# Kernel tuning notes

Hardware: AMD Instinct MI355X
Metric: run time of the kernel (lower is better)

Reference implementation:

```python
import jax, jax.numpy as jnp
import numpy as np

H = 8        # heads
DH = 64      # dim_head
IMG = 32     # image_size
KS = 5       # kernel_size (odd)
SCALE = DH ** -0.5


def _unfold(t, ks):
    # t: (b, c, Hp, Wp) already padded. Returns (b, c*ks*ks, Ho*Wo) with
    # channel-major layout (c outermost, then kh, kw) matching torch F.unfold.
    b, c, Hp, Wp = t.shape
    Ho, Wo = Hp - ks + 1, Wp - ks + 1
    pat = jnp.stack([t[:, :, i:i + Ho, j:j + Wo]
                     for i in range(ks) for j in range(ks)], axis=2)  # (b,c,ks*ks,Ho,Wo)
    return pat.reshape(b, c * ks * ks, Ho * Wo)


def setup_inputs() -> dict:
    key = jax.random.key(0)
    k1, k2, k3, k4 = jax.random.split(key, 4)
    b, n, dim, inner = 2, 1152, 512, 512
    x = jax.random.normal(k1, (b, n, dim), jnp.float32)
    w_qkv = jax.random.normal(k2, (dim, inner * 3), jnp.float32) * 0.02
    w_out = jax.random.normal(k3, (inner, dim), jnp.float32) * 0.02
    b_out = jax.random.normal(k4, (dim,), jnp.float32) * 0.02
    return {"x": x, "w_qkv": w_qkv, "w_out": w_out, "b_out": b_out}


def reference(x, w_qkv, w_out, b_out):
    b, n, dim = x.shape
    img_len = IMG * IMG
    text_len = n - img_len
    NEG = -jnp.finfo(x.dtype).max

    qkv = x @ w_qkv                                   # (b, n, 3*inner)
    q, k, v = jnp.split(qkv, 3, axis=-1)

    def to_heads(t):
        return t.reshape(b, n, H, DH).transpose(0, 2, 1, 3).reshape(b * H, n, DH)

    q = to_heads(q) * SCALE
    k = to_heads(k)
    v = to_heads(v)

    # faithful to source: text slice is t[:, img_seq_len:], image is t[:, -img_seq_len:]
    q_text, q_img = q[:, img_len:], q[:, -img_len:]
    k_text, k_img = k[:, img_len:], k[:, -img_len:]
    v_text, v_img = v[:, img_len:], v[:, -img_len:]

    # ---- text branch. NOTE: source uses non-inplace masked_fill, so the
    # causal mask has NO effect -> plain softmax (faithful reproduction).
    dots_text = jnp.einsum('bid,bjd->bij', q_text, k_text)
    attn_text = jax.nn.softmax(dots_text, axis=-1)
    out_text = jnp.einsum('bij,bjd->bid', attn_text, v_text)

    # ---- image branch: local window via unfold
    def to_loc(t):
        g = t.transpose(0, 2, 1).reshape(b * H, DH, IMG, IMG)
        p = KS // 2
        g = jnp.pad(g, ((0, 0), (0, 0), (p, p), (p, p)))
        u = _unfold(g, KS)  # (bh, DH*KS*KS, img_len), channel-major (d outer)
        # faithful to source rearrange 'b (j d) i -> b i j d' (j outermost),
        # which regroups the channel-major unfold output.
        return u.reshape(b * H, KS * KS, DH, img_len).transpose(0, 3, 1, 2)

    k_loc = to_loc(k_img)  # (bh, img_len, KS*KS, DH)
    v_loc = to_loc(v_img)

    dots_txt = jnp.einsum('bid,bjd->bij', q_img, k_text)     # (bh, img_len, text_len)
    dots_loc = jnp.einsum('bid,bijd->bij', q_img, k_loc)     # (bh, img_len, KS*KS)

    # per-query key index mask (padded positions get index img_len -> never masked)
    p = KS // 2
    idx = jnp.arange(img_len, dtype=jnp.float32).reshape(1, 1, IMG, IMG)
    idx = jnp.pad(idx, ((0, 0), (0, 0), (p, p), (p, p)), constant_values=float(img_len))
    kidx = _unfold(idx, KS).transpose(0, 2, 1)               # (1, img_len, KS*KS)
    qidx = jnp.arange(img_len, dtype=jnp.float32).reshape(1, -1, 1)
    mask_loc = qidx <= kidx                                  # faithful: keep q <= k
    dots_loc = jnp.where(mask_loc, dots_loc, NEG)

    dots_img = jnp.concatenate([dots_txt, dots_loc], axis=-1)
    attn_img = jax.nn.softmax(dots_img, axis=-1)
    out_img = (jnp.einsum('bij,bjd->bid', attn_img[..., :text_len], v_text)
               + jnp.einsum('bij,bijd->bid', attn_img[..., text_len:], v_loc))

    out = jnp.concatenate([out_text, out_img], axis=1)       # (bh, n, DH)
    out = out.reshape(b, H, n, DH).transpose(0, 2, 1, 3).reshape(b, n, H * DH)
    return out @ w_out + b_out
```

## Files before the change

kernel.cpp:

```cpp
#include <hip/hip_runtime.h>
#include <hip/hip_bf16.h>
#include <math.h>

#define NTOK 1152
#define DIM 512
#define NQKV 1536
#define DHEAD 64
#define NBH 16
#define TEXTN 128
#define IMGLEN 1024
#define SEG (NBH * NTOK * DHEAD)
#define STF 68
#define TSTATE_F (NBH * IMGLEN * STF)
#define LPAD 40
#define KTSZ (NBH * TEXTN * DHEAD)

typedef __attribute__((ext_vector_type(8))) short bf16x8;
typedef __attribute__((ext_vector_type(4))) float f32x4;

__device__ __forceinline__ ushort f2bf(float f) {
    unsigned u = __float_as_uint(f);
    unsigned r = (u + 0x7FFFu + ((u >> 16) & 1u)) >> 16;
    return (ushort)r;
}
__device__ __forceinline__ float bf2f(ushort u) {
    return __uint_as_float(((unsigned)u) << 16);
}

__global__ __launch_bounds__(256) void prep_x_k(const float* __restrict__ X,
                                                ushort* __restrict__ xhi,
                                                ushort* __restrict__ xlo) {
    int i = (blockIdx.x * 256 + threadIdx.x) * 4;
    float4 v = *(const float4*)(X + i);
    ushort4 h, l;
    h.x = f2bf(v.x); l.x = f2bf(v.x - bf2f(h.x));
    h.y = f2bf(v.y); l.y = f2bf(v.y - bf2f(h.y));
    h.z = f2bf(v.z); l.z = f2bf(v.z - bf2f(h.z));
    h.w = f2bf(v.w); l.w = f2bf(v.w - bf2f(h.w));
    *(ushort4*)(xhi + i) = h;
    *(ushort4*)(xlo + i) = l;
}

__global__ __launch_bounds__(256) void prep_wt_k(const float* __restrict__ W,
                                                 ushort* __restrict__ thi,
                                                 ushort* __restrict__ tlo,
                                                 int K, int N) {
    __shared__ float tile[32][33];
    const int bx = blockIdx.x, by = blockIdx.y;
    const int c = threadIdx.x & 31, r8 = threadIdx.x >> 5;
#pragma unroll
    for (int i = 0; i < 4; ++i) {
        int rr = r8 + i * 8;
        tile[rr][c] = W[(size_t)(by * 32 + rr) * N + bx * 32 + c];
    }
    __syncthreads();
#pragma unroll
    for (int i = 0; i < 4; ++i) {
        int rr = r8 + i * 8;
        float v = tile[c][rr];
        size_t o = (size_t)(bx * 32 + rr) * K + by * 32 + c;
        ushort h = f2bf(v);
        thi[o] = h;
        tlo[o] = f2bf(v - bf2f(h));
    }
}

__global__ __launch_bounds__(256) void gemm_qkv_mfma(const ushort* __restrict__ xhi,
                                                     const ushort* __restrict__ xlo,
                                                     const ushort* __restrict__ wthi,
                                                     const ushort* __restrict__ wtlo,
                                                     float* __restrict__ qh,
                                                     float* __restrict__ kh,
                                                     float* __restrict__ vh,
                                                     ushort* __restrict__ qhi,
                                                     ushort* __restrict__ qlo,
                                                     ushort* __restrict__ kthi,
                                                     ushort* __restrict__ ktlo,
                                                     ushort* __restrict__ vthi,
                                                     ushort* __restrict__ vtlo) {
    __shared__ __align__(16) ushort Ah[128 * LPAD], Al[128 * LPAD];
    __shared__ __align__(16) ushort Bh[64 * LPAD], Bl[64 * LPAD];
    const int tid = threadIdx.x;
    const int lane = tid & 63;
    const int w = tid >> 6;
    const int wm = w >> 1, wn = w & 1;
    const int row0 = blockIdx.y * 128;
    const int col0 = blockIdx.x * 64;

    f32x4 acc[4][2];
#pragma unroll
    for (int a = 0; a < 4; ++a)
#pragma unroll
        for (int b = 0; b < 2; ++b) acc[a][b] = (f32x4){0.f, 0.f, 0.f, 0.f};

    const int arow = tid >> 1;
    const int akb = (tid & 1) * 16;
    const int brow = tid >> 2;
    const int bkb = (tid & 3) * 8;
    const int kf = (lane >> 4) * 8;
    const int lr = lane & 15;

    for (int k0 = 0; k0 < DIM; k0 += 32) {
        {
            const size_t g = (size_t)(row0 + arow) * DIM + k0 + akb;
            *(bf16x8*)&Ah[arow * LPAD + akb] = *(const bf16x8*)(xhi + g);
            *(bf16x8*)&Ah[arow * LPAD + akb + 8] = *(const bf16x8*)(xhi + g + 8);
            *(bf16x8*)&Al[arow * LPAD + akb] = *(const bf16x8*)(xlo + g);
            *(bf16x8*)&Al[arow * LPAD + akb + 8] = *(const bf16x8*)(xlo + g + 8);
        }
        {
            const size_t g = (size_t)(col0 + brow) * DIM + k0 + bkb;
            *(bf16x8*)&Bh[brow * LPAD + bkb] = *(const bf16x8*)(wthi + g);
            *(bf16x8*)&Bl[brow * LPAD + bkb] = *(const bf16x8*)(wtlo + g);
        }
        __syncthreads();
        bf16x8 ah[4], al[4], bh[2], bl[2];
#pragma unroll
        for (int mi = 0; mi < 4; ++mi) {
            int rr = wm * 64 + mi * 16 + lr;
            ah[mi] = *(const bf16x8*)&Ah[rr * LPAD + kf];
            al[mi] = *(const bf16x8*)&Al[rr * LPAD + kf];
        }
#pragma unroll
        for (int ni = 0; ni < 2; ++ni) {
            int rr = wn * 32 + ni * 16 + lr;
            bh[ni] = *(const bf16x8*)&Bh[rr * LPAD + kf];
            bl[ni] = *(const bf16x8*)&Bl[rr * LPAD + kf];
        }
#pragma unroll
        for (int mi = 0; mi < 4; ++mi)
#pragma unroll
            for (int ni = 0; ni < 2; ++ni) {
                acc[mi][ni] = __builtin_amdgcn_mfma_f32_16x16x32_bf16(ah[mi], bh[ni], acc[mi][ni], 0, 0, 0);
                acc[mi][ni] = __builtin_amdgcn_mfma_f32_16x16x32_bf16(ah[mi], bl[ni], acc[mi][ni], 0, 0, 0);
                acc[mi][ni] = __builtin_amdgcn_mfma_f32_16x16x32_bf16(al[mi], bh[ni], acc[mi][ni], 0, 0, 0);
            }
        __syncthreads();
    }

    const int which = col0 >> 9;
    const int hh = (col0 & 511) >> 6;
    const float scale = (which == 0) ? 0.125f : 1.f;
    float* dst = (which == 0) ? qh : ((which == 1) ? kh : vh);
#pragma unroll
    for (int mi = 0; mi < 4; ++mi)
#pragma unroll
        for (int ni = 0; ni < 2; ++ni)
#pragma unroll
            for (int j = 0; j < 4; ++j) {
                int r = row0 + wm * 64 + mi * 16 + (lane >> 4) * 4 + j;
                int b_i = r / NTOK, tok = r - b_i * NTOK;
                int d = wn * 32 + ni * 16 + (lane & 15);
                int bhi = b_i * 8 + hh;
                float val = acc[mi][ni][j] * scale;
                dst[((size_t)bhi * NTOK + tok) * DHEAD + d] = val;
                if (which == 0) {
                    size_t qo = ((size_t)bhi * NTOK + tok) * DHEAD + d;
                    ushort h2 = f2bf(val);
                    qhi[qo] = h2;
                    qlo[qo] = f2bf(val - bf2f(h2));
                } else if (tok >= IMGLEN) {
                    int tr = tok - IMGLEN;
                    ushort h2 = f2bf(val);
                    ushort l2 = f2bf(val - bf2f(h2));
                    if (which == 1) {
                        size_t ko = ((size_t)bhi * TEXTN + tr) * DHEAD + d;
                        kthi[ko] = h2; ktlo[ko] = l2;
                    } else {
                        size_t vo = ((size_t)bhi * DHEAD + d) * TEXTN + tr;
                        vthi[vo] = h2; vtlo[vo] = l2;
                    }
                }
            }
}

__global__ __launch_bounds__(256) void attn_text_mfma(const ushort* __restrict__ qhi,
                                                      const ushort* __restrict__ qlo,
                                                      const ushort* __restrict__ kthi,
                                                      const ushort* __restrict__ ktlo,
                                                      const ushort* __restrict__ vthi,
                                                      const ushort* __restrict__ vtlo,
                                                      ushort* __restrict__ ahi,
                                                      ushort* __restrict__ alo,
                                                      float* __restrict__ tstate) {
    __shared__ __align__(16) ushort Phi[4][16][136];
    __shared__ __align__(16) ushort Plo[4][16][136];
    const int bh = blockIdx.x / 18;
    const int tile = blockIdx.x % 18;
    const int wave = threadIdx.x >> 6;
    const int lane = threadIdx.x & 63;
    const int lr = lane & 15, lg = lane >> 4;
    const int kf = lg * 8;
    const int qrow0 = tile * 64 + wave * 16;
    const int tok0 = (tile < 2 ? 1024 + tile * 64 : tile * 64) + wave * 16;

    bf16x8 qah[2], qal[2];
    {
        const size_t qb = ((size_t)bh * NTOK + tok0 + lr) * DHEAD;
#pragma unroll
        for (int c = 0; c < 2; ++c) {
            qah[c] = *(const bf16x8*)(qhi + qb + c * 32 + kf);
            qal[c] = *(const bf16x8*)(qlo + qb + c * 32 + kf);
        }
    }
    f32x4 s[8];
#pragma unroll
    for (int t = 0; t < 8; ++t) s[t] = (f32x4){0.f, 0.f, 0.f, 0.f};
#pragma unroll
    for (int t = 0; t < 8; ++t) {
        const size_t kb = ((size_t)bh * TEXTN + t * 16 + lr) * DHEAD;
#pragma unroll
        for (int c = 0; c < 2; ++c) {
            bf16x8 kbh = *(const bf16x8*)(kthi + kb + c * 32 + kf);
            bf16x8 kbl = *(const bf16x8*)(ktlo + kb + c * 32 + kf);
            s[t] = __builtin_amdgcn_mfma_f32_16x16x32_bf16(qah[c], kbh, s[t], 0, 0, 0);
            s[t] = __builtin_amdgcn_mfma_f32_16x16x32_bf16(qah[c], kbl, s[t], 0, 0, 0);
            s[t] = __builtin_amdgcn_mfma_f32_16x16x32_bf16(qal[c], kbh, s[t], 0, 0, 0);
        }
    }
    float mx[4], sm[4];
#pragma unroll
    for (int r = 0; r < 4; ++r) {
        float v = s[0][r];
#pragma unroll
        for (int t = 1; t < 8; ++t) v = fmaxf(v, s[t][r]);
        mx[r] = v;
    }
#pragma unroll
    for (int msk = 1; msk <= 8; msk <<= 1)
#pragma unroll
        for (int r = 0; r < 4; ++r) mx[r] = fmaxf(mx[r], __shfl_xor(mx[r], msk));
#pragma unroll
    for (int r = 0; r < 4; ++r) sm[r] = 0.f;
#pragma unroll
    for (int t = 0; t < 8; ++t)
#pragma unroll
        for (int r = 0; r < 4; ++r) {
            float p = __expf(s[t][r] - mx[r]);
            s[t][r] = p;
            sm[r] += p;
        }
#pragma unroll
    for (int msk = 1; msk <= 8; msk <<= 1)
#pragma unroll
        for (int r = 0; r < 4; ++r) sm[r] += __shfl_xor(sm[r], msk);
#pragma unroll
    for (int t = 0; t < 8; ++t)
#pragma unroll
        for (int r = 0; r < 4; ++r) {
            float p = s[t][r];
            ushort h = f2bf(p);
            Phi[wave][lg * 4 + r][t * 16 + lr] = h;
            Plo[wave][lg * 4 + r][t * 16 + lr] = f2bf(p - bf2f(h));
        }
    __syncthreads();
    f32x4 o[4];
#pragma unroll
    for (int dt = 0; dt < 4; ++dt) o[dt] = (f32x4){0.f, 0.f, 0.f, 0.f};
#pragma unroll
    for (int c = 0; c < 4; ++c) {
        bf16x8 pah = *(const bf16x8*)&Phi[wave][lr][c * 32 + kf];
        bf16x8 pal = *(const bf16x8*)&Plo[wave][lr][c * 32 + kf];
#pragma unroll
        for (int dt = 0; dt < 4; ++dt) {
            const size_t vb = ((size_t)bh * DHEAD + dt * 16 + lr) * TEXTN + c * 32 + kf;
            bf16x8 vbh = *(const bf16x8*)(vthi + vb);
            bf16x8 vbl = *(const bf16x8*)(vtlo + vb);
            o[dt] = __builtin_amdgcn_mfma_f32_16x16x32_bf16(pah, vbh, o[dt], 0, 0, 0);
            o[dt] = __builtin_amdgcn_mfma_f32_16x16x32_bf16(pah, vbl, o[dt], 0, 0, 0);
            o[dt] = __builtin_amdgcn_mfma_f32_16x16x32_bf16(pal, vbh, o[dt], 0, 0, 0);
        }
    }
    if (tile < 2) {
#pragma unroll
        for (int r = 0; r < 4; ++r) {
            const int row = qrow0 + lg * 4 + r;
            const float inv = 1.f / sm[r];
            const size_t base = ((size_t)bh * NTOK + row) * DHEAD;
#pragma unroll
            for (int dt = 0; dt < 4; ++dt) {
                float v = o[dt][r] * inv;
                ushort h = f2bf(v);
                ahi[base + dt * 16 + lr] = h;
                alo[base + dt * 16 + lr] = f2bf(v - bf2f(h));
            }
        }
    } else {
#pragma unroll
        for (int r = 0; r < 4; ++r) {
            const int imgq = qrow0 - TEXTN + lg * 4 + r;
            float* st = tstate + ((size_t)bh * IMGLEN + imgq) * STF;
#pragma unroll
            for (int dt = 0; dt < 4; ++dt) st[dt * 16 + lr] = o[dt][r];
            if (lr == 0) { st[64] = mx[r]; st[65] = sm[r]; }
        }
    }
}

template <int W8>
__device__ inline void loc_dots8(const float* __restrict__ kimg, int y, int x,
                                 const float (&q)[64], float (&sd)[25]) {
#pragma unroll
    for (int t = 0; t < 25; ++t) {
        const int ny = y + t / 5 - 2;
        const int nx = x + t % 5 - 2;
        if (ny >= 0 && ny < 32 && nx >= 0 && nx < 32) {
            const float* kp = kimg + (size_t)(ny * 32 + nx) * DHEAD + W8 * 8;
            float4 k0 = *(const float4*)kp;
            float4 k1 = *(const float4*)(kp + 4);
            float ke[8] = {k0.x, k0.y, k0.z, k0.w, k1.x, k1.y, k1.z, k1.w};
#pragma unroll
            for (int e = 0; e < 8; ++e) {
                const int d = W8 * 8 + e;
                const int id2 = d * 25 + t;
                sd[id2 >> 6] += q[id2 & 63] * ke[e];
            }
        }
    }
}

template <int W, int T0, int T1>
__device__ inline void loc_pvr(const float* __restrict__ vimg, int y, int x,
                               const float (&p)[25], float (&po)[64]) {
#pragma unroll
    for (int t = T0; t < T1; ++t) {
        const int ny = y + t / 5 - 2;
        const int nx = x + t % 5 - 2;
        if (ny >= 0 && ny < 32 && nx >= 0 && nx < 32) {
            const float* vp = vimg + (size_t)(ny * 32 + nx) * DHEAD + W * 16;
#pragma unroll
            for (int g = 0; g < 4; ++g) {
                float4 vv = *(const float4*)(vp + g * 4);
                float ve[4] = {vv.x, vv.y, vv.z, vv.w};
#pragma unroll
                for (int e = 0; e < 4; ++e) {
                    const int d = W * 16 + g * 4 + e;
                    const int id2 = d * 25 + t;
                    po[id2 & 63] += p[id2 >> 6] * ve[e];
                }
            }
        }
    }
}

__global__ __launch_bounds__(512) void attn_img_k(const float* __restrict__ qh,
                                                  const float* __restrict__ kh,
                                                  const float* __restrict__ vh,
                                                  ushort* __restrict__ ahi,
                                                  ushort* __restrict__ alo,
                                                  const float* __restrict__ tstate) {
    __shared__ __align__(16) float smem[8 * 64 * 26];
    float (*sdb)[64][26] = reinterpret_cast<float (*)[64][26]>(smem);
    float (*pob)[64][68] = reinterpret_cast<float (*)[64][68]>(smem);
    const int bh = blockIdx.x >> 4;
    const int qtile = (blockIdx.x & 15) << 6;
    const int wave = threadIdx.x >> 6;
    const int lane = threadIdx.x & 63;
    const int qq = qtile + lane;
    const int y = qq >> 5, x = qq & 31;
    const float* kimg = kh + (size_t)(bh * NTOK + TEXTN) * DHEAD;
    const float* vimg = vh + (size_t)(bh * NTOK + TEXTN) * DHEAD;
    const float* st = tstate + ((size_t)(bh * IMGLEN + qq)) * STF;

    float sd[25];
#pragma unroll
    for (int j = 0; j < 25; ++j) sd[j] = 0.f;
    {
        float q[64];
        const float* qp = qh + ((size_t)(bh * NTOK + TEXTN + qq)) * DHEAD;
#pragma unroll
        for (int g = 0; g < 16; ++g) {
            float4 v4 = *(const float4*)(qp + g * 4);
            q[g * 4] = v4.x; q[g * 4 + 1] = v4.y; q[g * 4 + 2] = v4.z; q[g * 4 + 3] = v4.w;
        }
        switch (wave) {
            case 0: loc_dots8<0>(kimg, y, x, q, sd); break;
            case 1: loc_dots8<1>(kimg, y, x, q, sd); break;
            case 2: loc_dots8<2>(kimg, y, x, q, sd); break;
            case 3: loc_dots8<3>(kimg, y, x, q, sd); break;
            case 4: loc_dots8<4>(kimg, y, x, q, sd); break;
            case 5: loc_dots8<5>(kimg, y, x, q, sd); break;
            case 6: loc_dots8<6>(kimg, y, x, q, sd); break;
            default: loc_dots8<7>(kimg, y, x, q, sd); break;
        }
    }
#pragma unroll
    for (int j = 0; j < 25; ++j) sdb[wave][lane][j] = sd[j];
    __syncthreads();

    float p[25];
#pragma unroll
    for (int j = 0; j < 25; ++j)
        p[j] = ((sdb[0][lane][j] + sdb[1][lane][j]) + (sdb[2][lane][j] + sdb[3][lane][j])) +
               ((sdb[4][lane][j] + sdb[5][lane][j]) + (sdb[6][lane][j] + sdb[7][lane][j]));
    float m = st[64], l = st[65];
    float mloc = -1e30f;
#pragma unroll
    for (int j = 0; j < 25; ++j) {
        const int my = y + j / 5 - 2;
        const int mx = x + j % 5 - 2;
        bool inb = (my >= 0 && my < 32 && mx >= 0 && mx < 32);
        bool keep = inb ? (qq <= my * 32 + mx) : true;
        p[j] = keep ? p[j] : -1e30f;
        mloc = fmaxf(mloc, p[j]);
    }
    const float M = fmaxf(m, mloc);
    const float cc = __expf(m - M);
    l *= cc;
#pragma unroll
    for (int j = 0; j < 25; ++j) {
        p[j] = __expf(p[j] - M);
        l += p[j];
    }
    const float inv = 1.f / l;

    float po[64];
#pragma unroll
    for (int o = 0; o < 64; ++o) po[o] = 0.f;
    switch (wave) {
        case 0: loc_pvr<0, 0, 13>(vimg, y, x, p, po); break;
        case 1: loc_pvr<1, 0, 13>(vimg, y, x, p, po); break;
        case 2: loc_pvr<2, 0, 13>(vimg, y, x, p, po); break;
        case 3: loc_pvr<3, 0, 13>(vimg, y, x, p, po); break;
        case 4: loc_pvr<0, 13, 25>(vimg, y, x, p, po); break;
        case 5: loc_pvr<1, 13, 25>(vimg, y, x, p, po); break;
        case 6: loc_pvr<2, 13, 25>(vimg, y, x, p, po); break;
        default: loc_pvr<3, 13, 25>(vimg, y, x, p, po); break;
    }
    __syncthreads();

    if (wave < 2) {
#pragma unroll
        for (int o = 0; o < 64; ++o) pob[wave][lane][o] = po[o];
    }
    __syncthreads();
    if (wave >= 2 && wave < 4) {
#pragma unroll
        for (int o = 0; o < 64; ++o) pob[wave - 2][lane][o] += po[o];
    }
    __syncthreads();
    if (wave >= 4 && wave < 6) {
#pragma unroll
        for (int o = 0; o < 64; ++o) pob[wave - 4][lane][o] += po[o];
    }
    __syncthreads();
    if (wave >= 6) {
#pragma unroll
        for (int o = 0; o < 64; ++o) pob[wave - 6][lane][o] += po[o];
    }
    __syncthreads();

    if (wave < 4) {
        const float* stq = st + wave * 16;
        size_t base = ((size_t)(bh * NTOK + TEXTN + qq)) * DHEAD + wave * 16;
#pragma unroll
        for (int g = 0; g < 4; ++g) {
            float4 tv = *(const float4*)(stq + g * 4);
            float4 a0 = *(const float4*)&pob[0][lane][wave * 16 + g * 4];
            float4 a1 = *(const float4*)&pob[1][lane][wave * 16 + g * 4];
            float v0 = (a0.x + a1.x + cc * tv.x) * inv;
            float v1 = (a0.y + a1.y + cc * tv.y) * inv;
            float v2 = (a0.z + a1.z + cc * tv.z) * inv;
            float v3 = (a0.w + a1.w + cc * tv.w) * inv;
            ushort4 oh, ol;
            oh.x = f2bf(v0); ol.x = f2bf(v0 - bf2f(oh.x));
            oh.y = f2bf(v1); ol.y = f2bf(v1 - bf2f(oh.y));
            oh.z = f2bf(v2); ol.z = f2bf(v2 - bf2f(oh.z));
            oh.w = f2bf(v3); ol.w = f2bf(v3 - bf2f(oh.w));
            *(ushort4*)(ahi + base + g * 4) = oh;
            *(ushort4*)(alo + base + g * 4) = ol;
        }
    }
}

__global__ __launch_bounds__(256) void gemm_out_mfma(const ushort* __restrict__ ahi,
                                                     const ushort* __restrict__ alo,
                                                     const ushort* __restrict__ wthi,
                                                     const ushort* __restrict__ wtlo,
                                                     const float* __restrict__ bias,
                                                     float* __restrict__ Y) {
    __shared__ __align__(16) ushort Ah[128 * LPAD], Al[128 * LPAD];
    __shared__ __align__(16) ushort Bh[64 * LPAD], Bl[64 * LPAD];
    const int tid = threadIdx.x;
    const int lane = tid & 63;
    const int w = tid >> 6;
    const int wm = w >> 1, wn = w & 1;
    const int row0 = blockIdx.y * 128;
    const int col0 = blockIdx.x * 64;

    f32x4 acc[4][2];
#pragma unroll
    for (int a = 0; a < 4; ++a)
#pragma unroll
        for (int b = 0; b < 2; ++b) acc[a][b] = (f32x4){0.f, 0.f, 0.f, 0.f};

    const int arow = tid >> 1;
    const int akb = (tid & 1) * 16;
    const int brow = tid >> 2;
    const int bkb = (tid & 3) * 8;
    const int kf = (lane >> 4) * 8;
    const int lr = lane & 15;

    const int ar = row0 + arow;
    const int a_bi = ar / NTOK;
    const int a_tok = ar - a_bi * NTOK;

    for (int k0 = 0; k0 < DIM; k0 += 32) {
        {
            const int kg = k0 + akb;
            const int hh = kg >> 6, d0 = kg & 63;
            const size_t g = ((size_t)(a_bi * 8 + hh) * NTOK + a_tok) * DHEAD + d0;
            *(bf16x8*)&Ah[arow * LPAD + akb] = *(const bf16x8*)(ahi + g);
            *(bf16x8*)&Ah[arow * LPAD + akb + 8] = *(const bf16x8*)(ahi + g + 8);
            *(bf16x8*)&Al[arow * LPAD + akb] = *(const bf16x8*)(alo + g);
            *(bf16x8*)&Al[arow * LPAD + akb + 8] = *(const bf16x8*)(alo + g + 8);
        }
        {
            const size_t g = (size_t)(col0 + brow) * DIM + k0 + bkb;
            *(bf16x8*)&Bh[brow * LPAD + bkb] = *(const bf16x8*)(wthi + g);
            *(bf16x8*)&Bl[brow * LPAD + bkb] = *(const bf16x8*)(wtlo + g);
        }
        __syncthreads();
        bf16x8 ah[4], al[4], bh[2], bl[2];
#pragma unroll
        for (int mi = 0; mi < 4; ++mi) {
            int rr = wm * 64 + mi * 16 + lr;
            ah[mi] = *(const bf16x8*)&Ah[rr * LPAD + kf];
            al[mi] = *(const bf16x8*)&Al[rr * LPAD + kf];
        }
#pragma unroll
        for (int ni = 0; ni < 2; ++ni) {
            int rr = wn * 32 + ni * 16 + lr;
            bh[ni] = *(const bf16x8*)&Bh[rr * LPAD + kf];
            bl[ni] = *(const bf16x8*)&Bl[rr * LPAD + kf];
        }
#pragma unroll
        for (int mi = 0; mi < 4; ++mi)
#pragma unroll
            for (int ni = 0; ni < 2; ++ni) {
                acc[mi][ni] = __builtin_amdgcn_mfma_f32_16x16x32_bf16(ah[mi], bh[ni], acc[mi][ni], 0, 0, 0);
                acc[mi][ni] = __builtin_amdgcn_mfma_f32_16x16x32_bf16(ah[mi], bl[ni], acc[mi][ni], 0, 0, 0);
                acc[mi][ni] = __builtin_amdgcn_mfma_f32_16x16x32_bf16(al[mi], bh[ni], acc[mi][ni], 0, 0, 0);
            }
        __syncthreads();
    }

#pragma unroll
    for (int mi = 0; mi < 4; ++mi)
#pragma unroll
        for (int ni = 0; ni < 2; ++ni) {
            int cidx = col0 + wn * 32 + ni * 16 + (lane & 15);
            float bv = bias[cidx];
#pragma unroll
            for (int j = 0; j < 4; ++j) {
                int r = row0 + wm * 64 + mi * 16 + (lane >> 4) * 4 + j;
                Y[(size_t)r * DIM + cidx] = acc[mi][ni][j] + bv;
            }
        }
}

extern "C" void kernel_launch(void* const* d_in, const int* in_sizes, int n_in,
                              void* d_out, int out_size, void* d_ws, size_t ws_size,
                              hipStream_t stream) {
    const float* x = (const float*)d_in[0];
    const float* w_qkv = (const float*)d_in[1];
    const float* w_out = (const float*)d_in[2];
    const float* b_out = (const float*)d_in[3];
    float* Y = (float*)d_out;
    float* ws = (float*)d_ws;
    float* qh = ws;
    float* kh = ws + (size_t)SEG;
    float* vh = ws + 2 * (size_t)SEG;
    float* tstate = ws + 3 * (size_t)SEG;
    ushort* xhi = (ushort*)(ws + 3 * (size_t)SEG + TSTATE_F);
    ushort* xlo = xhi + (size_t)SEG;
    ushort* ahi = xhi;
    ushort* alo = xlo;
    ushort* wqthi = xlo + (size_t)SEG;
    ushort* wqtlo = wqthi + (size_t)DIM * NQKV;
    ushort* wothi = wqtlo + (size_t)DIM * NQKV;
    ushort* wotlo = wothi + (size_t)DIM * DIM;
    ushort* qhi = wotlo + (size_t)DIM * DIM;
    ushort* qlo = qhi + (size_t)SEG;
    ushort* kthi = qlo + (size_t)SEG;
    ushort* ktlo = kthi + (size_t)KTSZ;
    ushort* vthi = ktlo + (size_t)KTSZ;
    ushort* vtlo = vthi + (size_t)KTSZ;

    hipLaunchKernelGGL(prep_x_k, dim3(SEG / 1024), dim3(256), 0, stream, x, xhi, xlo);
    hipLaunchKernelGGL(prep_wt_k, dim3(NQKV / 32, DIM / 32), dim3(256), 0, stream,
                       w_qkv, wqthi, wqtlo, DIM, NQKV);
    hipLaunchKernelGGL(prep_wt_k, dim3(DIM / 32, DIM / 32), dim3(256), 0, stream,
                       w_out, wothi, wotlo, DIM, DIM);
    hipLaunchKernelGGL(gemm_qkv_mfma, dim3(NQKV / 64, 2304 / 128), dim3(256), 0, stream,
                       xhi, xlo, wqthi, wqtlo, qh, kh, vh,
                       qhi, qlo, kthi, ktlo, vthi, vtlo);
    hipLaunchKernelGGL(attn_text_mfma, dim3(NBH * 18), dim3(256), 0, stream,
                       qhi, qlo, kthi, ktlo, vthi, vtlo, ahi, alo, tstate);
    hipLaunchKernelGGL(attn_img_k, dim3(NBH * 16), dim3(512), 0, stream,
                       qh, kh, vh, ahi, alo, tstate);
    hipLaunchKernelGGL(gemm_out_mfma, dim3(DIM / 64, 2304 / 128), dim3(256), 0, stream,
                       ahi, alo, wothi, wotlo, b_out, Y);
}
```

Measured before the change: 133.6 us.

## Stage local-window K/V halo tiles in swizzled LDS for image attention

The image local-attention kernel now cooperatively loads a 6-row halo of K and V (192 pixels) plus the block's Q tile into shared memory, using an XOR swizzle to avoid bank conflicts. The window dot products and PV accumulation then read from LDS instead of re-reading global memory for each of the 25 neighbours. This removes redundant global and cache traffic. In exchange, LDS use grows to roughly 150KB per block, so launch bounds are pinned to one block per CU, which reduces occupancy.

```diff
diff --git a/kernel.cpp b/kernel.cpp
--- a/kernel.cpp
+++ b/kernel.cpp
@@ -298,16 +298,17 @@
 }
 
 template <int W8>
-__device__ inline void loc_dots8(const float* __restrict__ kimg, int y, int x,
-                                 const float (&q)[64], float (&sd)[25]) {
+__device__ inline void loc_dots8_lds(const float* __restrict__ Kl, int yloc, int x, int y,
+                                     const float (&q)[64], float (&sd)[25]) {
 #pragma unroll
     for (int t = 0; t < 25; ++t) {
         const int ny = y + t / 5 - 2;
         const int nx = x + t % 5 - 2;
         if (ny >= 0 && ny < 32 && nx >= 0 && nx < 32) {
-            const float* kp = kimg + (size_t)(ny * 32 + nx) * DHEAD + W8 * 8;
-            float4 k0 = *(const float4*)kp;
-            float4 k1 = *(const float4*)(kp + 4);
+            const int px = (yloc + t / 5) * 32 + nx;
+            const float* base = Kl + px * 64;
+            float4 k0 = *(const float4*)(base + (((2 * W8) ^ (px & 7)) << 2));
+            float4 k1 = *(const float4*)(base + (((2 * W8 + 1) ^ (px & 7)) << 2));
             float ke[8] = {k0.x, k0.y, k0.z, k0.w, k1.x, k1.y, k1.z, k1.w};
 #pragma unroll
             for (int e = 0; e < 8; ++e) {
@@ -320,69 +321,97 @@
 }
 
 template <int W, int T0, int T1>
-__device__ inline void loc_pvr(const float* __restrict__ vimg, int y, int x,
-                               const float (&p)[25], float (&po)[64]) {
+__device__ inline void loc_pvr_lds(const float* __restrict__ Vl, int yloc, int x, int y,
+                                   const float (&pp)[25], float (&po)[64]) {
 #pragma unroll
     for (int t = T0; t < T1; ++t) {
         const int ny = y + t / 5 - 2;
         const int nx = x + t % 5 - 2;
         if (ny >= 0 && ny < 32 && nx >= 0 && nx < 32) {
-            const float* vp = vimg + (size_t)(ny * 32 + nx) * DHEAD + W * 16;
+            const int px = (yloc + t / 5) * 32 + nx;
+            const float* base = Vl + px * 64;
 #pragma unroll
             for (int g = 0; g < 4; ++g) {
-                float4 vv = *(const float4*)(vp + g * 4);
+                float4 vv = *(const float4*)(base + (((4 * W + g) ^ (px & 7)) << 2));
                 float ve[4] = {vv.x, vv.y, vv.z, vv.w};
 #pragma unroll
                 for (int e = 0; e < 4; ++e) {
                     const int d = W * 16 + g * 4 + e;
                     const int id2 = d * 25 + t;
-                    po[id2 & 63] += p[id2 >> 6] * ve[e];
+                    po[id2 & 63] += pp[id2 >> 6] * ve[e];
                 }
             }
         }
     }
 }
 
-__global__ __launch_bounds__(512) void attn_img_k(const float* __restrict__ qh,
-                                                  const float* __restrict__ kh,
-                                                  const float* __restrict__ vh,
-                                                  ushort* __restrict__ ahi,
-                                                  ushort* __restrict__ alo,
-                                                  const float* __restrict__ tstate) {
+__global__ __launch_bounds__(512, 1) void attn_img_k(const float* __restrict__ qh,
+                                                     const float* __restrict__ kh,
+                                                     const float* __restrict__ vh,
+                                                     ushort* __restrict__ ahi,
+                                                     ushort* __restrict__ alo,
+                                                     const float* __restrict__ tstate) {
     __shared__ __align__(16) float smem[8 * 64 * 26];
+    __shared__ __align__(16) float Kl[192 * 64];
+    __shared__ __align__(16) float Vl[192 * 64];
     float (*sdb)[64][26] = reinterpret_cast<float (*)[64][26]>(smem);
     float (*pob)[64][68] = reinterpret_cast<float (*)[64][68]>(smem);
     const int bh = blockIdx.x >> 4;
     const int qtile = (blockIdx.x & 15) << 6;
+    const int yr0 = qtile >> 5;
     const int wave = threadIdx.x >> 6;
     const int lane = threadIdx.x & 63;
     const int qq = qtile + lane;
     const int y = qq >> 5, x = qq & 31;
+    const int yloc = lane >> 5;
     const float* kimg = kh + (size_t)(bh * NTOK + TEXTN) * DHEAD;
     const float* vimg = vh + (size_t)(bh * NTOK + TEXTN) * DHEAD;
     const float* st = tstate + ((size_t)(bh * IMGLEN + qq)) * STF;
 
+#pragma unroll
+    for (int i = 0; i < 6; ++i) {
+        int flat = threadIdx.x + i * 512;
+        int px = flat >> 4, b = flat & 15;
+        int gy = yr0 - 2 + (px >> 5), gx = px & 31;
+        if (gy >= 0 && gy < 32) {
+            size_t off = ((size_t)(gy * 32 + gx)) * DHEAD + b * 4;
+            int dsto = px * 64 + ((b ^ (px & 7)) << 2);
+            *(float4*)&Kl[dsto] = *(const float4*)(kimg + off);
+            *(float4*)&Vl[dsto] = *(const float4*)(vimg + off);
+        }
+    }
+    {
+        const float* qbase = qh + ((size_t)(bh * NTOK + TEXTN + qtile)) * DHEAD;
+#pragma unroll
+        for (int i = 0; i < 2; ++i) {
+            int flat = threadIdx.x + i * 512;
+            int px = flat >> 4, b = flat & 15;
+            *(float4*)&smem[px * 64 + ((b ^ (px & 7)) << 2)] =
+                *(const float4*)(qbase + (size_t)px * DHEAD + b * 4);
+        }
+    }
+    __syncthreads();
+
+    float q[64];
+#pragma unroll
+    for (int b = 0; b < 16; ++b) {
+        float4 v = *(const float4*)&smem[lane * 64 + ((b ^ (lane & 7)) << 2)];
+        q[b * 4] = v.x; q[b * 4 + 1] = v.y; q[b * 4 + 2] = v.z; q[b * 4 + 3] = v.w;
+    }
+    __syncthreads();
+
     float sd[25];
 #pragma unroll
     for (int j = 0; j < 25; ++j) sd[j] = 0.f;
-    {
-        float q[64];
-        const float* qp = qh + ((size_t)(bh * NTOK + TEXTN + qq)) * DHEAD;
-#pragma unroll
-        for (int g = 0; g < 16; ++g) {
-            float4 v4 = *(const float4*)(qp + g * 4);
-            q[g * 4] = v4.x; q[g * 4 + 1] = v4.y; q[g * 4 + 2] = v4.z; q[g * 4 + 3] = v4.w;
-        }
-        switch (wave) {
-            case 0: loc_dots8<0>(kimg, y, x, q, sd); break;
-            case 1: loc_dots8<1>(kimg, y, x, q, sd); break;
-            case 2: loc_dots8<2>(kimg, y, x, q, sd); break;
-            case 3: loc_dots8<3>(kimg, y, x, q, sd); break;
-            case 4: loc_dots8<4>(kimg, y, x, q, sd); break;
-            case 5: loc_dots8<5>(kimg, y, x, q, sd); break;
-            case 6: loc_dots8<6>(kimg, y, x, q, sd); break;
-            default: loc_dots8<7>(kimg, y, x, q, sd); break;
-        }
+    switch (wave) {
+        case 0: loc_dots8_lds<0>(Kl, yloc, x, y, q, sd); break;
+        case 1: loc_dots8_lds<1>(Kl, yloc, x, y, q, sd); break;
+        case 2: loc_dots8_lds<2>(Kl, yloc, x, y, q, sd); break;
+        case 3: loc_dots8_lds<3>(Kl, yloc, x, y, q, sd); break;
+        case 4: loc_dots8_lds<4>(Kl, yloc, x, y, q, sd); break;
+        case 5: loc_dots8_lds<5>(Kl, yloc, x, y, q, sd); break;
+        case 6: loc_dots8_lds<6>(Kl, yloc, x, y, q, sd); break;
+        default: loc_dots8_lds<7>(Kl, yloc, x, y, q, sd); break;
     }
 #pragma unroll
     for (int j = 0; j < 25; ++j) sdb[wave][lane][j] = sd[j];
@@ -398,9 +427,9 @@
 #pragma unroll
     for (int j = 0; j < 25; ++j) {
         const int my = y + j / 5 - 2;
-        const int mx = x + j % 5 - 2;
-        bool inb = (my >= 0 && my < 32 && mx >= 0 && mx < 32);
-        bool keep = inb ? (qq <= my * 32 + mx) : true;
+        const int mx2 = x + j % 5 - 2;
+        bool inb = (my >= 0 && my < 32 && mx2 >= 0 && mx2 < 32);
+        bool keep = inb ? (qq <= my * 32 + mx2) : true;
         p[j] = keep ? p[j] : -1e30f;
         mloc = fmaxf(mloc, p[j]);
     }
@@ -418,14 +447,14 @@
 #pragma unroll
     for (int o = 0; o < 64; ++o) po[o] = 0.f;
     switch (wave) {
-        case 0: loc_pvr<0, 0, 13>(vimg, y, x, p, po); break;
-        case 1: loc_pvr<1, 0, 13>(vimg, y, x, p, po); break;
-        case 2: loc_pvr<2, 0, 13>(vimg, y, x, p, po); break;
-        case 3: loc_pvr<3, 0, 13>(vimg, y, x, p, po); break;
-        case 4: loc_pvr<0, 13, 25>(vimg, y, x, p, po); break;
-        case 5: loc_pvr<1, 13, 25>(vimg, y, x, p, po); break;
-        case 6: loc_pvr<2, 13, 25>(vimg, y, x, p, po); break;
-        default: loc_pvr<3, 13, 25>(vimg, y, x, p, po); break;
+        case 0: loc_pvr_lds<0, 0, 13>(Vl, yloc, x, y, p, po); break;
+        case 1: loc_pvr_lds<1, 0, 13>(Vl, yloc, x, y, p, po); break;
+        case 2: loc_pvr_lds<2, 0, 13>(Vl, yloc, x, y, p, po); break;
+        case 3: loc_pvr_lds<3, 0, 13>(Vl, yloc, x, y, p, po); break;
+        case 4: loc_pvr_lds<0, 13, 25>(Vl, yloc, x, y, p, po); break;
+        case 5: loc_pvr_lds<1, 13, 25>(Vl, yloc, x, y, p, po); break;
+        case 6: loc_pvr_lds<2, 13, 25>(Vl, yloc, x, y, p, po); break;
+        default: loc_pvr_lds<3, 13, 25>(Vl, yloc, x, y, p, po); break;
     }
     __syncthreads();
 
```

After: 131.3 us. About the same (-1.8%).
